# Kernel tuning notes

Measured on AMD Instinct MI355X. Metric: run time of the kernel, lower is better.

Reference implementation:

```python
import jax, jax.numpy as jnp
import numpy as np

B, SEQ, D_MODEL, N_HEADS = 4, 4096, 1024, 16
HEAD_DIM = D_MODEL // N_HEADS


def setup_inputs() -> dict:
    key = jax.random.key(0)
    ks = jax.random.split(key, 12)
    d = D_MODEL
    s = 1.0 / np.sqrt(d)  # ~nn.Linear init scale
    f = lambda k, shape, sc=1.0: jax.random.normal(k, shape, dtype=jnp.float32) * sc
    return {
        "queries": f(ks[0], (B, SEQ, d)),
        "keys":    f(ks[1], (B, SEQ, d)),
        "values":  f(ks[2], (B, SEQ, d)),
        "Wr": f(ks[3], (d, d), s), "br": jnp.zeros((d,), jnp.float32),
        "Wk": f(ks[4], (d, d), s), "bk": jnp.zeros((d,), jnp.float32),
        "Wv": f(ks[5], (d, d), s), "bv": jnp.zeros((d,), jnp.float32),
        "Wo": f(ks[6], (d, d), s), "bo": jnp.zeros((d,), jnp.float32),
        "decay": f(ks[7], (N_HEADS, HEAD_DIM), 0.01) - 5.0,
        "bonus": jnp.zeros((N_HEADS, HEAD_DIM), jnp.float32),
    }


def reference(queries, keys, values, Wr, br, Wk, bk, Wv, bv, Wo, bo, decay, bonus):
    Bb, N, d = queries.shape
    M = keys.shape[1]
    H = decay.shape[0]
    Dh = d // H

    # projections (nn.Linear: x @ W^T + b), split into heads
    r = (queries @ Wr.T + br).reshape(Bb, N, H, Dh)              # (B,N,H,D)
    k = (keys    @ Wk.T + bk).reshape(Bb, M, H, Dh).transpose(1, 0, 2, 3)  # (M,B,H,D)
    v = (values  @ Wv.T + bv).reshape(Bb, M, H, Dh).transpose(1, 0, 2, 3)  # (M,B,H,D)

    decay_factor = jnp.exp(-jnp.exp(decay))  # exp(w), w = -exp(decay); (H,D)

    def step(carry, kv):
        num, den = carry                       # (B,H,D)
        k_t, v_t = kv                          # (B,H,D)
        kc = jnp.clip(k_t, -10.0, 10.0)
        ek = jnp.exp(kc)
        bonus_w = jnp.exp(bonus + kc)          # (B,H,D) via broadcast
        wkv_t = (num + bonus_w * v_t) / (den + bonus_w + 1e-6)
        num = num * decay_factor + ek * v_t
        den = den * decay_factor + ek
        return (num, den), wkv_t

    init = (jnp.zeros((Bb, H, Dh), queries.dtype), jnp.zeros((Bb, H, Dh), queries.dtype))
    _, wkv = jax.lax.scan(step, init, (k, v))   # (M,B,H,D); here M == N
    wkv = wkv[:N].transpose(1, 0, 2, 3)         # (B,N,H,D)

    out = (jax.nn.sigmoid(r) * wkv).reshape(Bb, N, d)
    return out @ Wo.T + bo
```

## Files before the change

kernel.cpp:

```cpp
#include <hip/hip_runtime.h>

#define T_SEQ   4096
#define DM      1024
#define NB      4
#define ROWS    (NB * T_SEQ)
#define NCH     64
#define LCH     (T_SEQ / NCH)

typedef unsigned short ushort_t;

typedef __attribute__((ext_vector_type(8))) short bf16x8;
typedef __attribute__((ext_vector_type(4))) float f32x4;

__device__ __forceinline__ float bf2f(ushort_t u) {
  return __uint_as_float(((unsigned int)u) << 16);
}
__device__ __forceinline__ ushort_t f2bf(float f) {
  unsigned int u = __float_as_uint(f);
  u += 0x7FFFu + ((u >> 16) & 1u);
  return (ushort_t)(u >> 16);
}
__device__ __forceinline__ unsigned cvtpk(float lo, float hi) {
  unsigned r;
  asm("v_cvt_pk_bf16_f32 %0, %1, %2" : "=v"(r) : "v"(lo), "v"(hi));
  return r;
}

__device__ __forceinline__ void async16(const void* g, void* l) {
  __builtin_amdgcn_global_load_lds(
      (const __attribute__((address_space(1))) unsigned int*)g,
      (__attribute__((address_space(3))) unsigned int*)l, 16, 0, 0);
}

__device__ __forceinline__ int fragoffB32(int row, int col) {
  int p = ((row >> 4) << 10) + ((row & 15) << 6) + (col << 1);
  return p ^ (((row >> 3) & 1) << 5);
}
__device__ __forceinline__ int fragoffA32f(int row, int col) {
  int p = ((row >> 3) << 10) + ((row & 7) << 7) + (col << 2);
  return p ^ ((row & 7) << 4);
}

__global__ __launch_bounds__(256)
void cvt_pack(const float* __restrict__ Wr, const float* __restrict__ Wk,
              const float* __restrict__ Wv, const float* __restrict__ Wo,
              const float* __restrict__ br, const float* __restrict__ bk,
              const float* __restrict__ bv, const float* __restrict__ bo,
              ushort_t* __restrict__ wb, float* __restrict__ biasP) {
  const int bid = blockIdx.x;
  if (bid < 2048) {
    const int n4 = (DM * DM);
    for (int i = bid * 256 + threadIdx.x; i < n4; i += 2048 * 256) {
      const int seg = i >> 18;
      const float* src = seg == 0 ? Wr : seg == 1 ? Wk : seg == 2 ? Wv : Wo;
      const float4 f = ((const float4*)src)[i & 262143];
      ushort4 o;
      o.x = f2bf(f.x); o.y = f2bf(f.y); o.z = f2bf(f.z); o.w = f2bf(f.w);
      ((ushort4*)wb)[i] = o;
    }
  } else {
    const int s = bid - 2048;
    const float* b = s == 0 ? br : s == 1 ? bk : s == 2 ? bv : bo;
    for (int i = threadIdx.x; i < DM; i += 256) biasP[s * DM + i] = b[i];
  }
}

template <typename AT, typename OutT, int GROUPS>
__global__ __launch_bounds__(512, 2)
void gemm3(const AT* __restrict__ A0, const AT* __restrict__ A1,
           const AT* __restrict__ A2, const ushort_t* __restrict__ Wb,
           const float* __restrict__ biasP, OutT* __restrict__ Cb,
           const int M, const int N, const int K) {
  constexpr bool A_F32 = sizeof(AT) == 4;
  constexpr int ABYTES = A_F32 ? 32768 : 16384;
  constexpr int BBYTES = 16384;
  constexpr int AL = A_F32 ? 4 : 2;
  __shared__ char smem[3 * (ABYTES + BBYTES)];

  const int T = K >> 5;
  const int ntpg = (M >> 8) * (N >> 8);
  const int nwg  = GROUPS * ntpg;
  const int wg   = ((int)blockIdx.x & 7) * (nwg >> 3) + ((int)blockIdx.x >> 3);
  const int g     = wg / ntpg;
  const int local = wg % ntpg;
  const int ntn = N >> 8;
  const int tm = local / ntn, tn = local % ntn;
  const int m0 = tm << 8, n0 = tn << 8;
  const AT*       Ag   = g == 0 ? A0 : (g == 1 ? A1 : A2);
  const ushort_t* W    = Wb + (size_t)g * N * K;
  const float*    bias = biasP + g * N;
  OutT*           C    = Cb + (size_t)g * M * N;

  const int tid  = threadIdx.x;
  const int lane = tid & 63;
  const int wave = tid >> 6;
  const int wm128 = (wave >> 2) * 128;
  const int wn64  = (wave & 3) * 64;
  const int r15 = lane & 15;
  const int kq8 = (lane >> 4) * 8;

  int arow[AL], acol[AL];
  #pragma unroll
  for (int rho = 0; rho < AL; ++rho) {
    const int p = rho * 8192 + tid * 16;
    if constexpr (A_F32) {
      arow[rho] = ((p >> 10) << 3) | ((p >> 7) & 7);
      acol[rho] = ((p ^ (((p >> 7) & 7) << 4)) >> 2) & 31;
    } else {
      const int e = (p ^ (((p >> 9) & 1) << 5)) >> 1;
      arow[rho] = ((e >> 9) << 4) | ((e >> 5) & 15);
      acol[rho] = e & 31;
    }
  }
  int brow[2], bcol[2];
  #pragma unroll
  for (int rho = 0; rho < 2; ++rho) {
    const int p = rho * 8192 + tid * 16;
    const int e = (p ^ (((p >> 9) & 1) << 5)) >> 1;
    brow[rho] = ((e >> 9) << 4) | ((e >> 5) & 15);
    bcol[rho] = e & 31;
  }

  auto stageA = [&](int tile) {
    const int boff = (tile % 3) * ABYTES;
    #pragma unroll
    for (int rho = 0; rho < AL; ++rho) {
      const AT* g2 = Ag + (size_t)(m0 + arow[rho]) * K + (tile << 5) + acol[rho];
      async16(g2, &smem[boff + rho * 8192 + tid * 16]);
    }
  };
  auto stageB = [&](int tile) {
    const int boff = 3 * ABYTES + (tile % 3) * BBYTES;
    #pragma unroll
    for (int rho = 0; rho < 2; ++rho) {
      const ushort_t* g2 = W + (size_t)(n0 + brow[rho]) * K + (tile << 5) + bcol[rho];
      async16(g2, &smem[boff + rho * 8192 + tid * 16]);
    }
  };

  auto rdAfrag = [&](int abase, int row) -> bf16x8 {
    if constexpr (A_F32) {
      const f32x4 lo = *(const f32x4*)&smem[abase + fragoffA32f(row, kq8)];
      const f32x4 hi = *(const f32x4*)&smem[abase + fragoffA32f(row, kq8 + 4)];
      union { uint4 u4; bf16x8 b; } cv;
      cv.u4.x = cvtpk(lo[0], lo[1]); cv.u4.y = cvtpk(lo[2], lo[3]);
      cv.u4.z = cvtpk(hi[0], hi[1]); cv.u4.w = cvtpk(hi[2], hi[3]);
      return cv.b;
    } else {
      return *(const bf16x8*)&smem[abase + fragoffB32(row, kq8)];
    }
  };

  f32x4 acc[8][4];
  #pragma unroll
  for (int i = 0; i < 8; ++i)
    #pragma unroll
    for (int j = 0; j < 4; ++j)
      acc[i][j] = (f32x4){0.f, 0.f, 0.f, 0.f};
  bf16x8 bfr[4];

  stageA(0); stageB(0); stageA(1); stageB(1);
  if constexpr (A_F32) asm volatile("s_waitcnt vmcnt(6)" ::: "memory");
  else                 asm volatile("s_waitcnt vmcnt(4)" ::: "memory");
  __builtin_amdgcn_s_barrier();

#define PH3(H, STG, TAILW)                                                       \
  {                                                                              \
    bf16x8 af[4];                                                                \
    _Pragma("unroll") for (int q = 0; q < 4; ++q)                                \
      af[q] = rdAfrag(curA, wm128 + (H) * 64 + q * 16 + r15);                    \
    if ((H) == 0) {                                                              \
      _Pragma("unroll") for (int fj = 0; fj < 4; ++fj)                           \
        bfr[fj] = *(const bf16x8*)&smem[curB +                                   \
            fragoffB32(wn64 + (fj << 4) + r15, kq8)];                            \
    }                                                                            \
    STG();                                                                       \
    __builtin_amdgcn_s_barrier();                                                \
    __builtin_amdgcn_s_setprio(1);                                               \
    _Pragma("unroll") for (int q = 0; q < 4; ++q)                                \
      _Pragma("unroll") for (int fj = 0; fj < 4; ++fj)                           \
        acc[(H) * 4 + q][fj] = __builtin_amdgcn_mfma_f32_16x16x32_bf16(          \
            af[q], bfr[fj], acc[(H) * 4 + q][fj], 0, 0, 0);                      \
    __builtin_amdgcn_s_setprio(0);                                               \
    TAILW();                                                                     \
    __builtin_amdgcn_s_barrier();                                                \
  }

  for (int j = 0; j < T; ++j) {
    const int curA = (j % 3) * ABYTES;
    const int curB = 3 * ABYTES + (j % 3) * BBYTES;
    const bool p1 = (j + 1 < T), p2 = (j + 2 < T);
    auto sA = [&] { if (p2) stageA(j + 2); };
    auto sB = [&] { if (p2) stageB(j + 2); };
    auto nw = [&] {};
    auto tw = [&] {
      if (!p1) return;
      if (p2) {
        if constexpr (A_F32) asm volatile("s_waitcnt vmcnt(6)" ::: "memory");
        else                 asm volatile("s_waitcnt vmcnt(4)" ::: "memory");
      } else {
        asm volatile("s_waitcnt vmcnt(0)" ::: "memory");
      }
    };
    PH3(0, sA, nw);
    PH3(1, sB, tw);
  }
#undef PH3

  float bias4[4];
  #pragma unroll
  for (int fj = 0; fj < 4; ++fj) bias4[fj] = bias[n0 + wn64 + fj * 16 + r15];
  #pragma unroll
  for (int fi = 0; fi < 8; ++fi) {
    const int row0 = m0 + wm128 + fi * 16 + (lane >> 4) * 4;
    #pragma unroll
    for (int fj = 0; fj < 4; ++fj) {
      const int col = n0 + wn64 + fj * 16 + r15;
      #pragma unroll
      for (int r = 0; r < 4; ++r) {
        const float v = acc[fi][fj][r] + bias4[fj];
        if constexpr (sizeof(OutT) == 2) C[(size_t)(row0 + r) * N + col] = f2bf(v);
        else                             C[(size_t)(row0 + r) * N + col] = v;
      }
    }
  }
}

__global__ __launch_bounds__(256)
void wkv_pass1(const ushort_t* __restrict__ kp, const ushort_t* __restrict__ vp,
               const float* __restrict__ decay,
               float* __restrict__ s_num, float* __restrict__ s_den) {
  const int tid = threadIdx.x;
  const int grp = blockIdx.x & 3;
  const int c   = (blockIdx.x >> 2) & (NCH - 1);
  const int b   = (int)blockIdx.x >> 8;
  const int ch  = grp * 256 + tid;
  const float df = __expf(-__expf(decay[ch]));
  size_t idx = (size_t)b * T_SEQ * DM + (size_t)(c * LCH) * DM + ch;
  float num = 0.f, den = 0.f;
  for (int u = 0; u < LCH; ++u, idx += DM) {
    float kf = bf2f(kp[idx]);
    kf = fminf(fmaxf(kf, -10.f), 10.f);
    const float ek = __expf(kf);
    const float vv = bf2f(vp[idx]);
    num = fmaf(num, df, ek * vv);
    den = fmaf(den, df, ek);
  }
  const size_t si = ((size_t)b * NCH + c) * DM + ch;
  s_num[si] = num;
  s_den[si] = den;
}

__global__ __launch_bounds__(256)
void wkv_pass2(const float* __restrict__ decay,
               float* __restrict__ s_num, float* __restrict__ s_den) {
  const int tid = threadIdx.x;
  const int grp = blockIdx.x & 3;
  const int b   = (int)blockIdx.x >> 2;
  const int ch  = grp * 256 + tid;
  const float dfL = __expf(-__expf(decay[ch]) * (float)LCH);
  float an = 0.f, ad = 0.f;
  size_t si = (size_t)b * NCH * DM + ch;
  for (int c = 0; c < NCH; ++c, si += DM) {
    const float ln = s_num[si], ld = s_den[si];
    s_num[si] = an; s_den[si] = ad;
    an = fmaf(an, dfL, ln);
    ad = fmaf(ad, dfL, ld);
  }
}

__global__ __launch_bounds__(256)
void wkv_pass3(const ushort_t* __restrict__ kp, const ushort_t* __restrict__ vp,
               ushort_t* rg, const float* __restrict__ decay,
               const float* __restrict__ bonus,
               const float* __restrict__ s_num, const float* __restrict__ s_den) {
  const int tid = threadIdx.x;
  const int grp = blockIdx.x & 3;
  const int c   = (blockIdx.x >> 2) & (NCH - 1);
  const int b   = (int)blockIdx.x >> 8;
  const int ch  = grp * 256 + tid;
  const float df = __expf(-__expf(decay[ch]));
  const float eb = __expf(bonus[ch]);
  const size_t si = ((size_t)b * NCH + c) * DM + ch;
  float num = s_num[si], den = s_den[si];
  size_t idx = (size_t)b * T_SEQ * DM + (size_t)(c * LCH) * DM + ch;
  for (int u = 0; u < LCH; ++u, idx += DM) {
    float kf = bf2f(kp[idx]);
    kf = fminf(fmaxf(kf, -10.f), 10.f);
    const float ek = __expf(kf);
    const float bw = eb * ek;
    const float vv = bf2f(vp[idx]);
    const float rr = bf2f(rg[idx]);
    const float numer = fmaf(bw, vv, num);
    const float denom = den + bw + 1e-6f;
    const float wkv = numer * __builtin_amdgcn_rcpf(denom);
    const float sig = __builtin_amdgcn_rcpf(1.f + __expf(-rr));
    rg[idx] = f2bf(sig * wkv);
    num = fmaf(num, df, ek * vv);
    den = fmaf(den, df, ek);
  }
}

extern "C" void kernel_launch(void* const* d_in, const int* in_sizes, int n_in,
                              void* d_out, int out_size, void* d_ws, size_t ws_size,
                              hipStream_t stream) {
  const float* q   = (const float*)d_in[0];
  const float* ky  = (const float*)d_in[1];
  const float* vl  = (const float*)d_in[2];
  const float* Wr  = (const float*)d_in[3];
  const float* br  = (const float*)d_in[4];
  const float* Wk  = (const float*)d_in[5];
  const float* bk  = (const float*)d_in[6];
  const float* Wv  = (const float*)d_in[7];
  const float* bv  = (const float*)d_in[8];
  const float* Wo  = (const float*)d_in[9];
  const float* bo  = (const float*)d_in[10];
  const float* decay = (const float*)d_in[11];
  const float* bonus = (const float*)d_in[12];
  float* out = (float*)d_out;

  const size_t NE = (size_t)ROWS * DM;
  const size_t WE = (size_t)DM * DM;

  ushort_t* wb = (ushort_t*)d_ws;
  float* biasP = (float*)(wb + 4 * WE);
  ushort_t* rp = (ushort_t*)(biasP + 4 * DM);
  ushort_t* kp = rp + NE;
  ushort_t* vp = kp + NE;
  float* s_num = (float*)(vp + NE);
  float* s_den = s_num + (size_t)NB * NCH * DM;
  ushort_t* G  = rp;

  dim3 cB(256);
  dim3 gemmBlk(512);
  dim3 projGrid(3 * (ROWS / 256) * (DM / 256));
  dim3 gemmGrid((ROWS / 256) * (DM / 256));
  dim3 scanGrid(NB * NCH * (DM / 256)), scanBlk(256);

  cvt_pack<<<dim3(2052), cB, 0, stream>>>(Wr, Wk, Wv, Wo, br, bk, bv, bo, wb, biasP);
  gemm3<float, ushort_t, 3><<<projGrid, gemmBlk, 0, stream>>>(
      q, ky, vl, wb, biasP, rp, ROWS, DM, DM);
  wkv_pass1<<<scanGrid, scanBlk, 0, stream>>>(kp, vp, decay, s_num, s_den);
  wkv_pass2<<<dim3(NB * DM / 256), scanBlk, 0, stream>>>(decay, s_num, s_den);
  wkv_pass3<<<scanGrid, scanBlk, 0, stream>>>(kp, vp, rp, decay, bonus, s_num, s_den);
  gemm3<ushort_t, float, 1><<<gemmGrid, gemmBlk, 0, stream>>>(
      G, G, G, wb + 3 * WE, biasP + 3 * DM, out, ROWS, DM, DM);
}
```

Baseline: 254.4 us.

## Rewrite projection GEMM as 1024-thread kernel with register-staged fp32 A conversion

Replaces the templated projection GEMM with a dedicated 1024-thread kernel. It loads fp32 activations into registers three tiles ahead, converts them to bf16 once, and writes the result to a double-buffered LDS tile. Weights stream through a 4-deep async LDS ring. The old path staged fp32 A in LDS and converted it on every fragment read, so the new one halves A LDS traffic and footprint and drops the redundant conversions. The cost is more register pressure, one block per CU, and a barrier every k-step. The output GEMM is specialised into a bf16-only copy.

```diff
diff --git a/kernel.cpp b/kernel.cpp
--- a/kernel.cpp
+++ b/kernel.cpp
@@ -36,9 +36,9 @@
   int p = ((row >> 4) << 10) + ((row & 15) << 6) + (col << 1);
   return p ^ (((row >> 3) & 1) << 5);
 }
-__device__ __forceinline__ int fragoffA32f(int row, int col) {
-  int p = ((row >> 3) << 10) + ((row & 7) << 7) + (col << 2);
-  return p ^ ((row & 7) << 4);
+__device__ __forceinline__ int fragoff(int row, int col) {
+  int p = (((row >> 4) * 2 + (col >> 5)) << 10) + ((row & 15) << 6) + ((col & 31) << 1);
+  return p ^ (((row >> 3) & 1) << 5);
 }
 
 __global__ __launch_bounds__(256)
@@ -65,32 +65,142 @@
   }
 }
 
-template <typename AT, typename OutT, int GROUPS>
-__global__ __launch_bounds__(512, 2)
-void gemm3(const AT* __restrict__ A0, const AT* __restrict__ A1,
-           const AT* __restrict__ A2, const ushort_t* __restrict__ Wb,
-           const float* __restrict__ biasP, OutT* __restrict__ Cb,
-           const int M, const int N, const int K) {
-  constexpr bool A_F32 = sizeof(AT) == 4;
-  constexpr int ABYTES = A_F32 ? 32768 : 16384;
-  constexpr int BBYTES = 16384;
-  constexpr int AL = A_F32 ? 4 : 2;
-  __shared__ char smem[3 * (ABYTES + BBYTES)];
-
+__global__ __launch_bounds__(1024)
+void proj1024(const float* __restrict__ Aq, const float* __restrict__ Ak,
+              const float* __restrict__ Av, const ushort_t* __restrict__ Wb,
+              const float* __restrict__ biasP, ushort_t* __restrict__ Cb,
+              const int M, const int N, const int K) {
+  __shared__ char smem[98304];
   const int T = K >> 5;
   const int ntpg = (M >> 8) * (N >> 8);
-  const int nwg  = GROUPS * ntpg;
-  const int wg   = ((int)blockIdx.x & 7) * (nwg >> 3) + ((int)blockIdx.x >> 3);
+  const int nwg  = 3 * ntpg;
+  const int wg = ((int)blockIdx.x & 7) * (nwg >> 3) + ((int)blockIdx.x >> 3);
   const int g     = wg / ntpg;
   const int local = wg % ntpg;
   const int ntn = N >> 8;
   const int tm = local / ntn, tn = local % ntn;
   const int m0 = tm << 8, n0 = tn << 8;
-  const AT*       Ag   = g == 0 ? A0 : (g == 1 ? A1 : A2);
+  const float*    Af   = g == 0 ? Aq : (g == 1 ? Ak : Av);
   const ushort_t* W    = Wb + (size_t)g * N * K;
   const float*    bias = biasP + g * N;
-  OutT*           C    = Cb + (size_t)g * M * N;
-
+  ushort_t*       C    = Cb + (size_t)g * M * N;
+
+  const int tid  = threadIdx.x;
+  const int lane = tid & 63;
+  const int wave = tid >> 6;
+  const int wr = (wave >> 2) * 64;
+  const int wc = (wave & 3) * 64;
+  const int r15 = lane & 15;
+  const int kq8 = (lane >> 4) * 8;
+
+  int srow, scol;
+  {
+    const int p = tid * 16;
+    const int e = (p ^ (((p >> 9) & 1) << 5)) >> 1;
+    srow = ((e >> 9) << 4) | ((e >> 5) & 15);
+    scol = e & 31;
+  }
+  const float*    aSrc = Af + (size_t)(m0 + srow) * K + scol;
+  const ushort_t* bSrc = W  + (size_t)(n0 + srow) * K + scol;
+
+  float4 rA0[2], rA1[2], rA2[2];
+
+#define ALOAD(BUF, t)                                                            \
+  { const float* s_ = aSrc + ((t) << 5);                                         \
+    BUF[0] = *(const float4*)s_; BUF[1] = *(const float4*)(s_ + 4); }
+#define BSTAGE(t)                                                                \
+  async16(bSrc + ((t) << 5), &smem[32768 + ((t) & 3) * 16384 + tid * 16]);
+#define ACVT(BUF, t)                                                             \
+  { uint4 w_;                                                                    \
+    w_.x = cvtpk(BUF[0].x, BUF[0].y); w_.y = cvtpk(BUF[0].z, BUF[0].w);          \
+    w_.z = cvtpk(BUF[1].x, BUF[1].y); w_.w = cvtpk(BUF[1].z, BUF[1].w);          \
+    *(uint4*)&smem[(((t) & 1) << 14) + tid * 16] = w_; }
+
+  f32x4 acc[4][4];
+  #pragma unroll
+  for (int i = 0; i < 4; ++i)
+    #pragma unroll
+    for (int j = 0; j < 4; ++j)
+      acc[i][j] = (f32x4){0.f, 0.f, 0.f, 0.f};
+
+  ALOAD(rA0, 0); BSTAGE(0);
+  ALOAD(rA1, 1); BSTAGE(1);
+  ALOAD(rA2, 2); BSTAGE(2);
+  ACVT(rA0, 0);
+  asm volatile("s_waitcnt vmcnt(6)" ::: "memory");
+  asm volatile("s_waitcnt lgkmcnt(0)" ::: "memory");
+  __builtin_amdgcn_s_barrier();
+
+#define PITER(J, BL, BC)                                                         \
+  {                                                                              \
+    const int j_ = (J);                                                          \
+    const bool pA = (j_ + 3 < T);                                                \
+    const bool pC = (j_ + 1 < T);                                                \
+    if (pA) { ALOAD(BL, j_ + 3); BSTAGE(j_ + 3); }                               \
+    if (pC) { ACVT(BC, j_ + 1); }                                                \
+    const int abase = (j_ & 1) << 14;                                            \
+    const int bbase = 32768 + (j_ & 3) * 16384;                                  \
+    bf16x8 bfr[4];                                                               \
+    _Pragma("unroll") for (int fj = 0; fj < 4; ++fj)                             \
+      bfr[fj] = *(const bf16x8*)&smem[bbase +                                    \
+          fragoffB32(wc + (fj << 4) + r15, kq8)];                                \
+    __builtin_amdgcn_s_setprio(1);                                               \
+    _Pragma("unroll") for (int q = 0; q < 4; ++q) {                              \
+      const bf16x8 af = *(const bf16x8*)&smem[abase +                            \
+          fragoffB32(wr + (q << 4) + r15, kq8)];                                 \
+      _Pragma("unroll") for (int fj = 0; fj < 4; ++fj)                           \
+        acc[q][fj] = __builtin_amdgcn_mfma_f32_16x16x32_bf16(                    \
+            af, bfr[fj], acc[q][fj], 0, 0, 0);                                   \
+    }                                                                            \
+    __builtin_amdgcn_s_setprio(0);                                               \
+    if (pA) asm volatile("s_waitcnt vmcnt(3)" ::: "memory");                     \
+    else    asm volatile("s_waitcnt vmcnt(0)" ::: "memory");                     \
+    asm volatile("s_waitcnt lgkmcnt(0)" ::: "memory");                           \
+    __builtin_amdgcn_s_barrier();                                                \
+  }
+
+  for (int jj = 0; jj + 3 <= T - 2; jj += 3) {
+    PITER(jj + 0, rA0, rA1);
+    PITER(jj + 1, rA1, rA2);
+    PITER(jj + 2, rA2, rA0);
+  }
+  PITER(T - 2, rA0, rA1);
+  PITER(T - 1, rA1, rA2);
+#undef PITER
+#undef ALOAD
+#undef BSTAGE
+#undef ACVT
+
+  float bias4[4];
+  #pragma unroll
+  for (int fj = 0; fj < 4; ++fj) bias4[fj] = bias[n0 + wc + fj * 16 + r15];
+  #pragma unroll
+  for (int fi = 0; fi < 4; ++fi) {
+    const int row0 = m0 + wr + fi * 16 + (lane >> 4) * 4;
+    #pragma unroll
+    for (int fj = 0; fj < 4; ++fj) {
+      const int col = n0 + wc + fj * 16 + r15;
+      #pragma unroll
+      for (int r = 0; r < 4; ++r)
+        C[(size_t)(row0 + r) * N + col] = f2bf(acc[fi][fj][r] + bias4[fj]);
+    }
+  }
+}
+
+template <typename OutT>
+__global__ __launch_bounds__(512, 2)
+void gemm3f(const ushort_t* __restrict__ A, const ushort_t* __restrict__ W,
+            const float* __restrict__ bias, OutT* __restrict__ C,
+            const int M, const int N, const int K) {
+  constexpr int ABYTES = 16384;
+  constexpr int BBYTES = 16384;
+  __shared__ char smem[3 * (ABYTES + BBYTES)];
+  const int T = K >> 5;
+  const int nwg = (M >> 8) * (N >> 8);
+  const int wg  = ((int)blockIdx.x & 7) * (nwg >> 3) + ((int)blockIdx.x >> 3);
+  const int ntn = N >> 8;
+  const int tm = wg / ntn, tn = wg % ntn;
+  const int m0 = tm << 8, n0 = tn << 8;
   const int tid  = threadIdx.x;
   const int lane = tid & 63;
   const int wave = tid >> 6;
@@ -99,33 +209,20 @@
   const int r15 = lane & 15;
   const int kq8 = (lane >> 4) * 8;
 
-  int arow[AL], acol[AL];
-  #pragma unroll
-  for (int rho = 0; rho < AL; ++rho) {
-    const int p = rho * 8192 + tid * 16;
-    if constexpr (A_F32) {
-      arow[rho] = ((p >> 10) << 3) | ((p >> 7) & 7);
-      acol[rho] = ((p ^ (((p >> 7) & 7) << 4)) >> 2) & 31;
-    } else {
-      const int e = (p ^ (((p >> 9) & 1) << 5)) >> 1;
-      arow[rho] = ((e >> 9) << 4) | ((e >> 5) & 15);
-      acol[rho] = e & 31;
-    }
-  }
-  int brow[2], bcol[2];
+  int arow[2], acol[2];
   #pragma unroll
   for (int rho = 0; rho < 2; ++rho) {
     const int p = rho * 8192 + tid * 16;
     const int e = (p ^ (((p >> 9) & 1) << 5)) >> 1;
-    brow[rho] = ((e >> 9) << 4) | ((e >> 5) & 15);
-    bcol[rho] = e & 31;
+    arow[rho] = ((e >> 9) << 4) | ((e >> 5) & 15);
+    acol[rho] = e & 31;
   }
 
   auto stageA = [&](int tile) {
     const int boff = (tile % 3) * ABYTES;
     #pragma unroll
-    for (int rho = 0; rho < AL; ++rho) {
-      const AT* g2 = Ag + (size_t)(m0 + arow[rho]) * K + (tile << 5) + acol[rho];
+    for (int rho = 0; rho < 2; ++rho) {
+      const ushort_t* g2 = A + (size_t)(m0 + arow[rho]) * K + (tile << 5) + acol[rho];
       async16(g2, &smem[boff + rho * 8192 + tid * 16]);
     }
   };
@@ -133,24 +230,11 @@
     const int boff = 3 * ABYTES + (tile % 3) * BBYTES;
     #pragma unroll
     for (int rho = 0; rho < 2; ++rho) {
-      const ushort_t* g2 = W + (size_t)(n0 + brow[rho]) * K + (tile << 5) + bcol[rho];
+      const ushort_t* g2 = W + (size_t)(n0 + arow[rho]) * K + (tile << 5) + acol[rho];
       async16(g2, &smem[boff + rho * 8192 + tid * 16]);
     }
   };
 
-  auto rdAfrag = [&](int abase, int row) -> bf16x8 {
-    if constexpr (A_F32) {
-      const f32x4 lo = *(const f32x4*)&smem[abase + fragoffA32f(row, kq8)];
-      const f32x4 hi = *(const f32x4*)&smem[abase + fragoffA32f(row, kq8 + 4)];
-      union { uint4 u4; bf16x8 b; } cv;
-      cv.u4.x = cvtpk(lo[0], lo[1]); cv.u4.y = cvtpk(lo[2], lo[3]);
-      cv.u4.z = cvtpk(hi[0], hi[1]); cv.u4.w = cvtpk(hi[2], hi[3]);
-      return cv.b;
-    } else {
-      return *(const bf16x8*)&smem[abase + fragoffB32(row, kq8)];
-    }
-  };
-
   f32x4 acc[8][4];
   #pragma unroll
   for (int i = 0; i < 8; ++i)
@@ -160,15 +244,15 @@
   bf16x8 bfr[4];
 
   stageA(0); stageB(0); stageA(1); stageB(1);
-  if constexpr (A_F32) asm volatile("s_waitcnt vmcnt(6)" ::: "memory");
-  else                 asm volatile("s_waitcnt vmcnt(4)" ::: "memory");
+  asm volatile("s_waitcnt vmcnt(4)" ::: "memory");
   __builtin_amdgcn_s_barrier();
 
 #define PH3(H, STG, TAILW)                                                       \
   {                                                                              \
     bf16x8 af[4];                                                                \
     _Pragma("unroll") for (int q = 0; q < 4; ++q)                                \
-      af[q] = rdAfrag(curA, wm128 + (H) * 64 + q * 16 + r15);                    \
+      af[q] = *(const bf16x8*)&smem[curA +                                       \
+          fragoffB32(wm128 + (H) * 64 + q * 16 + r15, kq8)];                     \
     if ((H) == 0) {                                                              \
       _Pragma("unroll") for (int fj = 0; fj < 4; ++fj)                           \
         bfr[fj] = *(const bf16x8*)&smem[curB +                                   \
@@ -195,12 +279,8 @@
     auto nw = [&] {};
     auto tw = [&] {
       if (!p1) return;
-      if (p2) {
-        if constexpr (A_F32) asm volatile("s_waitcnt vmcnt(6)" ::: "memory");
-        else                 asm volatile("s_waitcnt vmcnt(4)" ::: "memory");
-      } else {
-        asm volatile("s_waitcnt vmcnt(0)" ::: "memory");
-      }
+      if (p2) asm volatile("s_waitcnt vmcnt(4)" ::: "memory");
+      else    asm volatile("s_waitcnt vmcnt(0)" ::: "memory");
     };
     PH3(0, sA, nw);
     PH3(1, sB, tw);
@@ -332,17 +412,14 @@
   ushort_t* G  = rp;
 
   dim3 cB(256);
-  dim3 gemmBlk(512);
-  dim3 projGrid(3 * (ROWS / 256) * (DM / 256));
-  dim3 gemmGrid((ROWS / 256) * (DM / 256));
+  dim3 projGrid(3 * (ROWS / 256) * (DM / 256)), projBlk(1024);
+  dim3 gemmGrid((ROWS / 256) * (DM / 256)), gemmBlk(512);
   dim3 scanGrid(NB * NCH * (DM / 256)), scanBlk(256);
 
   cvt_pack<<<dim3(2052), cB, 0, stream>>>(Wr, Wk, Wv, Wo, br, bk, bv, bo, wb, biasP);
-  gemm3<float, ushort_t, 3><<<projGrid, gemmBlk, 0, stream>>>(
-      q, ky, vl, wb, biasP, rp, ROWS, DM, DM);
+  proj1024<<<projGrid, projBlk, 0, stream>>>(q, ky, vl, wb, biasP, rp, ROWS, DM, DM);
   wkv_pass1<<<scanGrid, scanBlk, 0, stream>>>(kp, vp, decay, s_num, s_den);
   wkv_pass2<<<dim3(NB * DM / 256), scanBlk, 0, stream>>>(decay, s_num, s_den);
   wkv_pass3<<<scanGrid, scanBlk, 0, stream>>>(kp, vp, rp, decay, bonus, s_num, s_den);
-  gemm3<ushort_t, float, 1><<<gemmGrid, gemmBlk, 0, stream>>>(
-      G, G, G, wb + 3 * WE, biasP + 3 * DM, out, ROWS, DM, DM);
-}
+  gemm3f<float><<<gemmGrid, gemmBlk, 0, stream>>>(G, wb + 3 * WE, biasP + 3 * DM, out, ROWS, DM, DM);
+}
```

Result: slower. 416.3 us (+63.6%).
